# Performance work log

Hardware: AMD Instinct MI355X
Metric: run time of the kernel (lower is better)

## Reference

```python
import jax, jax.numpy as jnp
import numpy as np

B, T, D = 4, 2048, 1024
H, HD = 16, 64  # n_heads, head_dim; H*HD == D

def setup_inputs() -> dict:
    key = jax.random.key(0)
    ks = jax.random.split(key, 9)
    s = 1.0 / np.sqrt(D)
    return {
        "x": jax.random.normal(ks[0], (B, T, D), dtype=jnp.float32),
        "Wq": jax.random.normal(ks[1], (D, D), dtype=jnp.float32) * s,
        "bq": jnp.zeros((D,), dtype=jnp.float32),
        "Wk": jax.random.normal(ks[2], (D, D), dtype=jnp.float32) * s,
        "bk": jnp.zeros((D,), dtype=jnp.float32),
        "Wv": jax.random.normal(ks[3], (D, D), dtype=jnp.float32) * s,
        "bv": jnp.zeros((D,), dtype=jnp.float32),
        "Wo": jax.random.normal(ks[4], (D, D), dtype=jnp.float32) * s,
        "bo": jnp.zeros((D,), dtype=jnp.float32),
    }

def reference(x, Wq, bq, Wk, bk, Wv, bv, Wo, bo):
    # Linear(in,out): y = x @ W.T + b (weights stored [out,in])
    q = (jnp.einsum('btd,ed->bte', x, Wq) + bq).reshape(B, T, H, HD).transpose(0, 2, 1, 3)
    k = (jnp.einsum('btd,ed->bte', x, Wk) + bk).reshape(B, T, H, HD).transpose(0, 2, 1, 3)
    v = (jnp.einsum('btd,ed->bte', x, Wv) + bv).reshape(B, T, H, HD).transpose(0, 2, 1, 3)
    scale = jnp.sqrt(jnp.asarray(HD, dtype=x.dtype))
    attn = jnp.einsum('bhqd,bhkd->bhqk', q, k) / scale  # [B,H,T,T]
    attn = jax.nn.softmax(attn, axis=-1)
    out = jnp.einsum('bhqk,bhkd->bhqd', attn, v)
    out = out.transpose(0, 2, 1, 3).reshape(B, T, H * HD)
    return jnp.einsum('bte,de->btd', out, Wo) + bo
```

## Files before the change

kernel.cpp:

```cpp
#include <hip/hip_runtime.h>
#include <hip/hip_bf16.h>

#define B_ 4
#define T_ 2048
#define D_ 1024
#define H_ 16
#define HD_ 64
#define M_ (B_ * T_)

typedef __attribute__((ext_vector_type(8))) short   s16x8;
typedef __attribute__((ext_vector_type(4))) short   s16x4;
typedef __attribute__((ext_vector_type(4))) float   f32x4;
typedef __attribute__((ext_vector_type(4))) float   fvec4;
typedef __attribute__((ext_vector_type(4))) unsigned short u16x4;

union U4 { u16x4 v; unsigned int w[2]; };
union P2 { s16x4 v; unsigned int w[2]; };

__device__ inline unsigned short f2bf(float f) {
    unsigned int u = __float_as_uint(f);
    return (unsigned short)((u + 0x7fffu + ((u >> 16) & 1u)) >> 16);
}

__device__ inline unsigned int pk_bf16(float a, float b) {
    unsigned int r;
    asm("v_cvt_pk_bf16_f32 %0, %1, %2" : "=v"(r) : "v"(a), "v"(b));
    return r;
}

__device__ inline f32x4 mfma32(s16x8 a, s16x8 b, f32x4 c) {
    return __builtin_amdgcn_mfma_f32_16x16x32_bf16(a, b, c, 0, 0, 0);
}

__device__ inline void gld16(const unsigned short* g, unsigned short* l) {
    __builtin_amdgcn_global_load_lds(
        (const __attribute__((address_space(1))) unsigned int*)g,
        (__attribute__((address_space(3))) unsigned int*)l, 16, 0, 0);
}

__global__ void cvt_all(const float* __restrict__ x,
                        const float* __restrict__ wq, const float* __restrict__ wk,
                        const float* __restrict__ wv, const float* __restrict__ wo,
                        unsigned short* __restrict__ xb, unsigned short* __restrict__ wcat) {
    const int bid = blockIdx.x;
    const float* src; unsigned short* dst; int off;
    if (bid < 8192)       { src = x;  dst = xb;                  off = bid; }
    else if (bid < 9216)  { src = wq; dst = wcat;                off = bid - 8192; }
    else if (bid < 10240) { src = wk; dst = wcat + 1 * 1048576;  off = bid - 9216; }
    else if (bid < 11264) { src = wv; dst = wcat + 2 * 1048576;  off = bid - 10240; }
    else                  { src = wo; dst = wcat + 3 * 1048576;  off = bid - 11264; }
    int i = off * 1024 + threadIdx.x * 4;
    fvec4 v = *(const fvec4*)(src + i);
    U4 o;
    o.w[0] = pk_bf16(v[0], v[1]);
    o.w[1] = pk_bf16(v[2], v[3]);
    *(u16x4*)(dst + i) = o.v;
}

#define GEMM_BODY(A_, W_, SWAPPED_)                                                \
    __shared__ __align__(16) unsigned short As[2][128 * 32];                       \
    __shared__ __align__(16) unsigned short Bs[2][128 * 32];                       \
    const int tid = threadIdx.x;                                                   \
    const int wave = tid >> 6, lane = tid & 63;                                    \
    const int quad = lane >> 4, l16 = lane & 15;                                   \
    const int wr = (wave >> 1) * 64, wc = (wave & 1) * 64;                         \
    f32x4 acc[4][4] = {};                                                          \
    {                                                                              \
        for (int i = 0; i < 2; ++i) {                                              \
            int idx = tid + i * 256;                                               \
            int row = idx >> 2, c8 = (idx & 3) * 8;                                \
            gld16(A_ + (size_t)(m0 + row) * 1024 + c8, As[0] + idx * 8);           \
            gld16(W_ + (size_t)(n0 + row) * 1024 + c8, Bs[0] + idx * 8);           \
        }                                                                          \
    }                                                                              \
    for (int c = 0; c < 32; ++c) {                                                 \
        __syncthreads();                                                           \
        if (c + 1 < 32) {                                                          \
            int kn = (c + 1) * 32, nb = (c + 1) & 1;                               \
            for (int i = 0; i < 2; ++i) {                                          \
                int idx = tid + i * 256;                                           \
                int row = idx >> 2, c8 = (idx & 3) * 8;                            \
                gld16(A_ + (size_t)(m0 + row) * 1024 + kn + c8, As[nb] + idx * 8); \
                gld16(W_ + (size_t)(n0 + row) * 1024 + kn + c8, Bs[nb] + idx * 8); \
            }                                                                      \
        }                                                                          \
        const unsigned short* Ac = As[c & 1];                                      \
        const unsigned short* Bc = Bs[c & 1];                                      \
        s16x8 af[4], bfr[4];                                                       \
        for (int i = 0; i < 4; ++i)                                                \
            af[i] = *(const s16x8*)(Ac + (wr + i * 16 + l16) * 32 + quad * 8);     \
        for (int j = 0; j < 4; ++j)                                                \
            bfr[j] = *(const s16x8*)(Bc + (wc + j * 16 + l16) * 32 + quad * 8);    \
        if (SWAPPED_) {                                                            \
            for (int i = 0; i < 4; ++i)                                            \
                for (int j = 0; j < 4; ++j)                                        \
                    acc[i][j] = mfma32(bfr[j], af[i], acc[i][j]);                  \
        } else {                                                                   \
            for (int i = 0; i < 4; ++i)                                            \
                for (int j = 0; j < 4; ++j)                                        \
                    acc[i][j] = mfma32(af[i], bfr[j], acc[i][j]);                  \
        }                                                                          \
    }

__global__ __launch_bounds__(256) void gemm_qkv(
    const unsigned short* __restrict__ A, const unsigned short* __restrict__ Wcat,
    const float* __restrict__ bq, const float* __restrict__ bk, const float* __restrict__ bv,
    unsigned short* __restrict__ Qb, unsigned short* __restrict__ Kb,
    unsigned short* __restrict__ Vt, float qscale) {
    const int proj = blockIdx.y >> 3;
    const int m0 = blockIdx.x * 128, n0 = (blockIdx.y & 7) * 128;
    const unsigned short* W = Wcat + (size_t)proj * 1048576;
    const float* bias = proj == 0 ? bq : (proj == 1 ? bk : bv);
    const bool swapped = (proj != 2);

    GEMM_BODY(A, W, swapped)

    if (proj == 2) {
        for (int i = 0; i < 4; ++i) {
            int mbase = m0 + wr + i * 16 + quad * 4;
            int b = mbase >> 11, t = mbase & (T_ - 1);
            for (int j = 0; j < 4; ++j) {
                int n = n0 + wc + j * 16 + l16;
                float bi = bias[n];
                int h = n >> 6, hd = n & 63;
                U4 o;
                o.w[0] = pk_bf16(acc[i][j][0] + bi, acc[i][j][1] + bi);
                o.w[1] = pk_bf16(acc[i][j][2] + bi, acc[i][j][3] + bi);
                *(u16x4*)(Vt + ((size_t)(b * H_ + h) * HD_ + hd) * T_ + t) = o.v;
            }
        }
    } else {
        const float scale = (proj == 0) ? qscale : 1.0f;
        unsigned short* outp = (proj == 0) ? Qb : Kb;
        for (int i = 0; i < 4; ++i) {
            int t = m0 + wr + i * 16 + l16;
            int b = t >> 11, tt = t & (T_ - 1);
            for (int j = 0; j < 4; ++j) {
                int nb = n0 + wc + j * 16 + quad * 4;
                fvec4 bi = *(const fvec4*)(bias + nb);
                int h = nb >> 6, hd = nb & 63;
                float v0 = (acc[i][j][0] + bi[0]) * scale;
                float v1 = (acc[i][j][1] + bi[1]) * scale;
                float v2 = (acc[i][j][2] + bi[2]) * scale;
                float v3 = (acc[i][j][3] + bi[3]) * scale;
                U4 o;
                o.w[0] = pk_bf16(v0, v1);
                o.w[1] = pk_bf16(v2, v3);
                *(u16x4*)(outp + ((size_t)(b * H_ + h) * T_ + tt) * HD_ + hd) = o.v;
            }
        }
    }
}

__global__ __launch_bounds__(256) void gemm_o(
    const unsigned short* __restrict__ A, const unsigned short* __restrict__ W,
    const float* __restrict__ bias, float* __restrict__ out) {
    const int m0 = blockIdx.x * 128, n0 = blockIdx.y * 128;

    GEMM_BODY(A, W, true)

    for (int i = 0; i < 4; ++i) {
        int m = m0 + wr + i * 16 + l16;
        for (int j = 0; j < 4; ++j) {
            int nb = n0 + wc + j * 16 + quad * 4;
            fvec4 bi = *(const fvec4*)(bias + nb);
            fvec4 o = acc[i][j] + bi;
            *(fvec4*)(out + (size_t)m * D_ + nb) = o;
        }
    }
}

__global__ __launch_bounds__(256) void attn(
    const unsigned short* __restrict__ Qb, const unsigned short* __restrict__ Kb,
    const unsigned short* __restrict__ Vt, unsigned short* __restrict__ Ob) {
    __shared__ __align__(16) unsigned short Ks[2 * 4096];
    __shared__ __align__(16) unsigned short Vs[2 * 4096];

    const int tid = threadIdx.x;
    const int wave = tid >> 6, lane = tid & 63;
    const int quad = lane >> 4, l16 = lane & 15;

    const int flat = blockIdx.y * 16 + blockIdx.x;
    const int wid  = (flat & 7) * 128 + (flat >> 3);
    const int qblk = wid & 15, bh = wid >> 4;
    const int b = bh >> 4, h = bh & 15;
    const int q0 = qblk * 128 + wave * 32;

    const unsigned short* Qp = Qb + (size_t)bh * T_ * HD_;
    const unsigned short* Kp = Kb + (size_t)bh * T_ * HD_;
    const unsigned short* Vp = Vt + (size_t)bh * HD_ * T_;

    s16x8 qf[2][2];
    for (int qt = 0; qt < 2; ++qt)
        for (int ds = 0; ds < 2; ++ds)
            qf[qt][ds] = *(const s16x8*)(Qp + (size_t)(q0 + qt * 16 + l16) * HD_ + ds * 32 + quad * 8);

    f32x4 accO[2][4] = {};
    f32x4 accL[2] = {};

    const s16x8 ones = {0x3F80, 0x3F80, 0x3F80, 0x3F80,
                        0x3F80, 0x3F80, 0x3F80, 0x3F80};

    const int r0 = tid >> 3,           cg0 = (tid & 7) ^ (r0 & 7);
    const int r1 = (tid + 256) >> 3,   cg1 = (tid & 7) ^ (r1 & 7);

    const int xk  = quad ^ (l16 & 7);
    const int kro = l16 * 64 + xk * 8;
    const int kro1 = l16 * 64 + (xk ^ 4) * 8;

    auto stage = [&](int k0, int bufS) {
        gld16(Kp + (size_t)(k0 + r0) * HD_ + cg0 * 8, Ks + bufS + tid * 8);
        gld16(Kp + (size_t)(k0 + r1) * HD_ + cg1 * 8, Ks + bufS + (tid + 256) * 8);
        gld16(Vp + (size_t)r0 * T_ + k0 + cg0 * 8, Vs + bufS + tid * 8);
        gld16(Vp + (size_t)r1 * T_ + k0 + cg1 * 8, Vs + bufS + (tid + 256) * 8);
    };

    stage(0, 0);

    for (int c = 0; c < T_ / 64; ++c) {
        __syncthreads();

        if (c + 1 < T_ / 64) stage((c + 1) * 64, ((c + 1) & 1) * 4096);

        const unsigned short* Kc = Ks + (c & 1) * 4096;
        const unsigned short* Vc = Vs + (c & 1) * 4096;

        f32x4 st[2][4] = {};
        __builtin_amdgcn_s_setprio(1);
        for (int kt = 0; kt < 4; ++kt) {
            s16x8 kf0 = *(const s16x8*)(Kc + kt * 1024 + kro);
            s16x8 kf1 = *(const s16x8*)(Kc + kt * 1024 + kro1);
            for (int qt = 0; qt < 2; ++qt) {
                st[qt][kt] = mfma32(kf0, qf[qt][0], st[qt][kt]);
                st[qt][kt] = mfma32(kf1, qf[qt][1], st[qt][kt]);
            }
        }
        __builtin_amdgcn_s_setprio(0);

        s16x4 pb[2][4];
        for (int qt = 0; qt < 2; ++qt) {
            for (int kt = 0; kt < 4; ++kt) {
                float p0 = __builtin_amdgcn_exp2f(st[qt][kt][0]);
                float p1 = __builtin_amdgcn_exp2f(st[qt][kt][1]);
                float p2 = __builtin_amdgcn_exp2f(st[qt][kt][2]);
                float p3 = __builtin_amdgcn_exp2f(st[qt][kt][3]);
                P2 pk;
                pk.w[0] = pk_bf16(p0, p1);
                pk.w[1] = pk_bf16(p2, p3);
                pb[qt][kt] = pk.v;
            }
        }

        __builtin_amdgcn_s_setprio(1);
        for (int u = 0; u < 2; ++u) {
            s16x8 pf0 = __builtin_shufflevector(pb[0][2 * u], pb[0][2 * u + 1],
                                                0, 1, 2, 3, 4, 5, 6, 7);
            s16x8 pf1 = __builtin_shufflevector(pb[1][2 * u], pb[1][2 * u + 1],
                                                0, 1, 2, 3, 4, 5, 6, 7);
            accL[0] = mfma32(ones, pf0, accL[0]);
            accL[1] = mfma32(ones, pf1, accL[1]);
            const int cA = 4 * u + (quad >> 1);
            for (int dt = 0; dt < 4; ++dt) {
                const unsigned short* vrow = Vc + (dt * 16 + l16) * 64 + (quad & 1) * 4;
                s16x4 vlo = *(const s16x4*)(vrow + ((cA       ^ (l16 & 7)) * 8));
                s16x4 vhi = *(const s16x4*)(vrow + (((cA + 2) ^ (l16 & 7)) * 8));
                s16x8 vf = __builtin_shufflevector(vlo, vhi, 0, 1, 2, 3, 4, 5, 6, 7);
                accO[0][dt] = mfma32(vf, pf0, accO[0][dt]);
                accO[1][dt] = mfma32(vf, pf1, accO[1][dt]);
            }
        }
        __builtin_amdgcn_s_setprio(0);
    }

    for (int qt = 0; qt < 2; ++qt) {
        float inv = 1.f / accL[qt][0];
        int t = q0 + qt * 16 + l16;
        for (int dt = 0; dt < 4; ++dt) {
            U4 o;
            o.w[0] = pk_bf16(accO[qt][dt][0] * inv, accO[qt][dt][1] * inv);
            o.w[1] = pk_bf16(accO[qt][dt][2] * inv, accO[qt][dt][3] * inv);
            *(u16x4*)(Ob + ((size_t)b * T_ + t) * D_ + h * 64 + dt * 16 + quad * 4) = o.v;
        }
    }
}

extern "C" void kernel_launch(void* const* d_in, const int* in_sizes, int n_in,
                              void* d_out, int out_size, void* d_ws, size_t ws_size,
                              hipStream_t stream) {
    const float* x  = (const float*)d_in[0];
    const float* Wq = (const float*)d_in[1];
    const float* bq = (const float*)d_in[2];
    const float* Wk = (const float*)d_in[3];
    const float* bk = (const float*)d_in[4];
    const float* Wv = (const float*)d_in[5];
    const float* bv = (const float*)d_in[6];
    const float* Wo = (const float*)d_in[7];
    const float* bo = (const float*)d_in[8];
    float* out = (float*)d_out;

    const size_t SZ = (size_t)M_ * D_ * sizeof(unsigned short);
    unsigned short* xb   = (unsigned short*)d_ws;
    unsigned short* Qb   = (unsigned short*)((char*)d_ws + 1 * SZ);
    unsigned short* Kb   = (unsigned short*)((char*)d_ws + 2 * SZ);
    unsigned short* Vbt  = (unsigned short*)((char*)d_ws + 3 * SZ);
    unsigned short* Wcat = (unsigned short*)((char*)d_ws + 4 * SZ);
    unsigned short* Ob   = xb;

    const float qscale = 1.4426950408889634f / 8.0f;

    dim3 blk(256);
    cvt_all<<<dim3(12288), blk, 0, stream>>>(x, Wq, Wk, Wv, Wo, xb, Wcat);
    gemm_qkv<<<dim3(M_ / 128, 24), blk, 0, stream>>>(xb, Wcat, bq, bk, bv, Qb, Kb, Vbt, qscale);
    attn<<<dim3(T_ / 128, B_ * H_), blk, 0, stream>>>(Qb, Kb, Vbt, Ob);
    gemm_o<<<dim3(M_ / 128, D_ / 128), blk, 0, stream>>>(Ob, Wcat + 3 * 1048576, bo, out);
}
```

Baseline: 316.2 us.

## Permute V^T token order so attention V fragments load as single 16-byte reads

The QKV GEMM epilogue now writes V^T with a permuted token index within each 32-token group, so the attention kernel's PV MFMA operand is one contiguous 16-byte LDS read instead of two 8-byte reads plus a shuffle. The attention loop also replaces the staging lambda with precomputed, incrementally advanced global pointers and starts each score MFMA chain from a constant zero. The aim is fewer LDS instructions and less address arithmetic in the inner loop. The gain depends on the permutation exactly matching the MFMA k-ordering of the P fragments; any mismatch would silently corrupt the output.

```diff
diff --git a/kernel.cpp b/kernel.cpp
--- a/kernel.cpp
+++ b/kernel.cpp
@@ -15,7 +15,7 @@
 typedef __attribute__((ext_vector_type(4))) unsigned short u16x4;
 
 union U4 { u16x4 v; unsigned int w[2]; };
-union P2 { s16x4 v; unsigned int w[2]; };
+union P8 { s16x8 v; unsigned int w[4]; };
 
 __device__ inline unsigned short f2bf(float f) {
     unsigned int u = __float_as_uint(f);
@@ -119,6 +119,7 @@
         for (int i = 0; i < 4; ++i) {
             int mbase = m0 + wr + i * 16 + quad * 4;
             int b = mbase >> 11, t = mbase & (T_ - 1);
+            int tp = (t & ~31) | (((t >> 2) & 3) << 3) | (((t >> 4) & 1) << 2);
             for (int j = 0; j < 4; ++j) {
                 int n = n0 + wc + j * 16 + l16;
                 float bi = bias[n];
@@ -126,7 +127,7 @@
                 U4 o;
                 o.w[0] = pk_bf16(acc[i][j][0] + bi, acc[i][j][1] + bi);
                 o.w[1] = pk_bf16(acc[i][j][2] + bi, acc[i][j][3] + bi);
-                *(u16x4*)(Vt + ((size_t)(b * H_ + h) * HD_ + hd) * T_ + t) = o.v;
+                *(u16x4*)(Vt + ((size_t)(b * H_ + h) * HD_ + hd) * T_ + tp) = o.v;
             }
         }
     } else {
@@ -197,6 +198,7 @@
 
     f32x4 accO[2][4] = {};
     f32x4 accL[2] = {};
+    const f32x4 fzero = {0.f, 0.f, 0.f, 0.f};
 
     const s16x8 ones = {0x3F80, 0x3F80, 0x3F80, 0x3F80,
                         0x3F80, 0x3F80, 0x3F80, 0x3F80};
@@ -204,70 +206,77 @@
     const int r0 = tid >> 3,           cg0 = (tid & 7) ^ (r0 & 7);
     const int r1 = (tid + 256) >> 3,   cg1 = (tid & 7) ^ (r1 & 7);
 
-    const int xk  = quad ^ (l16 & 7);
-    const int kro = l16 * 64 + xk * 8;
+    const unsigned short* kp0 = Kp + (size_t)r0 * HD_ + cg0 * 8;
+    const unsigned short* kp1 = Kp + (size_t)r1 * HD_ + cg1 * 8;
+    const unsigned short* vp0 = Vp + (size_t)r0 * T_ + cg0 * 8;
+    const unsigned short* vp1 = Vp + (size_t)r1 * T_ + cg1 * 8;
+
+    const int xk   = quad ^ (l16 & 7);
+    const int kro  = l16 * 64 + xk * 8;
     const int kro1 = l16 * 64 + (xk ^ 4) * 8;
-
-    auto stage = [&](int k0, int bufS) {
-        gld16(Kp + (size_t)(k0 + r0) * HD_ + cg0 * 8, Ks + bufS + tid * 8);
-        gld16(Kp + (size_t)(k0 + r1) * HD_ + cg1 * 8, Ks + bufS + (tid + 256) * 8);
-        gld16(Vp + (size_t)r0 * T_ + k0 + cg0 * 8, Vs + bufS + tid * 8);
-        gld16(Vp + (size_t)r1 * T_ + k0 + cg1 * 8, Vs + bufS + (tid + 256) * 8);
-    };
-
-    stage(0, 0);
+    const int vro0 = l16 * 64 + ((quad)     ^ (l16 & 7)) * 8;
+    const int vro1 = l16 * 64 + ((4 + quad) ^ (l16 & 7)) * 8;
+
+    gld16(kp0, Ks + tid * 8);  gld16(kp1, Ks + tid * 8 + 2048);
+    gld16(vp0, Vs + tid * 8);  gld16(vp1, Vs + tid * 8 + 2048);
+    kp0 += 64 * HD_; kp1 += 64 * HD_; vp0 += 64; vp1 += 64;
 
     for (int c = 0; c < T_ / 64; ++c) {
         __syncthreads();
 
-        if (c + 1 < T_ / 64) stage((c + 1) * 64, ((c + 1) & 1) * 4096);
+        if (c + 1 < T_ / 64) {
+            unsigned short* dK = Ks + ((c + 1) & 1) * 4096 + tid * 8;
+            unsigned short* dV = Vs + ((c + 1) & 1) * 4096 + tid * 8;
+            gld16(kp0, dK);  gld16(kp1, dK + 2048);
+            gld16(vp0, dV);  gld16(vp1, dV + 2048);
+            kp0 += 64 * HD_; kp1 += 64 * HD_; vp0 += 64; vp1 += 64;
+        }
 
         const unsigned short* Kc = Ks + (c & 1) * 4096;
         const unsigned short* Vc = Vs + (c & 1) * 4096;
 
-        f32x4 st[2][4] = {};
+        f32x4 st[2][4];
         __builtin_amdgcn_s_setprio(1);
         for (int kt = 0; kt < 4; ++kt) {
             s16x8 kf0 = *(const s16x8*)(Kc + kt * 1024 + kro);
             s16x8 kf1 = *(const s16x8*)(Kc + kt * 1024 + kro1);
-            for (int qt = 0; qt < 2; ++qt) {
-                st[qt][kt] = mfma32(kf0, qf[qt][0], st[qt][kt]);
-                st[qt][kt] = mfma32(kf1, qf[qt][1], st[qt][kt]);
+            st[0][kt] = mfma32(kf0, qf[0][0], fzero);
+            st[0][kt] = mfma32(kf1, qf[0][1], st[0][kt]);
+            st[1][kt] = mfma32(kf0, qf[1][0], fzero);
+            st[1][kt] = mfma32(kf1, qf[1][1], st[1][kt]);
+        }
+        __builtin_amdgcn_s_setprio(0);
+
+        s16x8 pf[2][2];
+        for (int qt = 0; qt < 2; ++qt)
+            for (int u = 0; u < 2; ++u) {
+                P8 pk;
+                for (int kk = 0; kk < 2; ++kk) {
+                    f32x4 s = st[qt][2 * u + kk];
+                    float p0 = __builtin_amdgcn_exp2f(s[0]);
+                    float p1 = __builtin_amdgcn_exp2f(s[1]);
+                    float p2 = __builtin_amdgcn_exp2f(s[2]);
+                    float p3 = __builtin_amdgcn_exp2f(s[3]);
+                    pk.w[2 * kk]     = pk_bf16(p0, p1);
+                    pk.w[2 * kk + 1] = pk_bf16(p2, p3);
+                }
+                pf[qt][u] = pk.v;
             }
-        }
-        __builtin_amdgcn_s_setprio(0);
-
-        s16x4 pb[2][4];
-        for (int qt = 0; qt < 2; ++qt) {
-            for (int kt = 0; kt < 4; ++kt) {
-                float p0 = __builtin_amdgcn_exp2f(st[qt][kt][0]);
-                float p1 = __builtin_amdgcn_exp2f(st[qt][kt][1]);
-                float p2 = __builtin_amdgcn_exp2f(st[qt][kt][2]);
-                float p3 = __builtin_amdgcn_exp2f(st[qt][kt][3]);
-                P2 pk;
-                pk.w[0] = pk_bf16(p0, p1);
-                pk.w[1] = pk_bf16(p2, p3);
-                pb[qt][kt] = pk.v;
-            }
-        }
 
         __builtin_amdgcn_s_setprio(1);
-        for (int u = 0; u < 2; ++u) {
-            s16x8 pf0 = __builtin_shufflevector(pb[0][2 * u], pb[0][2 * u + 1],
-                                                0, 1, 2, 3, 4, 5, 6, 7);
-            s16x8 pf1 = __builtin_shufflevector(pb[1][2 * u], pb[1][2 * u + 1],
-                                                0, 1, 2, 3, 4, 5, 6, 7);
-            accL[0] = mfma32(ones, pf0, accL[0]);
-            accL[1] = mfma32(ones, pf1, accL[1]);
-            const int cA = 4 * u + (quad >> 1);
-            for (int dt = 0; dt < 4; ++dt) {
-                const unsigned short* vrow = Vc + (dt * 16 + l16) * 64 + (quad & 1) * 4;
-                s16x4 vlo = *(const s16x4*)(vrow + ((cA       ^ (l16 & 7)) * 8));
-                s16x4 vhi = *(const s16x4*)(vrow + (((cA + 2) ^ (l16 & 7)) * 8));
-                s16x8 vf = __builtin_shufflevector(vlo, vhi, 0, 1, 2, 3, 4, 5, 6, 7);
-                accO[0][dt] = mfma32(vf, pf0, accO[0][dt]);
-                accO[1][dt] = mfma32(vf, pf1, accO[1][dt]);
-            }
+        accL[0] = mfma32(ones, pf[0][0], accL[0]);
+        accL[1] = mfma32(ones, pf[1][0], accL[1]);
+        for (int dt = 0; dt < 4; ++dt) {
+            s16x8 vf = *(const s16x8*)(Vc + vro0 + dt * 1024);
+            accO[0][dt] = mfma32(vf, pf[0][0], accO[0][dt]);
+            accO[1][dt] = mfma32(vf, pf[1][0], accO[1][dt]);
+        }
+        accL[0] = mfma32(ones, pf[0][1], accL[0]);
+        accL[1] = mfma32(ones, pf[1][1], accL[1]);
+        for (int dt = 0; dt < 4; ++dt) {
+            s16x8 vf = *(const s16x8*)(Vc + vro1 + dt * 1024);
+            accO[0][dt] = mfma32(vf, pf[0][1], accO[0][dt]);
+            accO[1][dt] = mfma32(vf, pf[1][1], accO[1][dt]);
         }
         __builtin_amdgcn_s_setprio(0);
     }
```

After: 307.0 us. -2.9%, faster.
